# Performance work log

Measured on AMD Instinct MI355X. Metric: run time of the kernel, lower is better.

## Reference

```python
import jax, jax.numpy as jnp
import numpy as np

VOCAB = 65
N_EMBD = 32
BLOCK = 8
N_HEADS = 4
HEAD = N_EMBD // N_HEADS  # 8
SQRT_C = float(N_EMBD) ** 0.5  # faithful bug: scores are MULTIPLIED by sqrt(n_embd)


def setup_inputs() -> dict:
    key = jax.random.key(0)
    ks = jax.random.split(key, 12)
    B, T = 65536, 8
    idx = jax.random.randint(ks[0], (B, T), 0, VOCAB, dtype=jnp.int64 if jax.config.jax_enable_x64 else jnp.int32)
    targets = jax.random.randint(ks[1], (B, T), 0, VOCAB, dtype=idx.dtype)
    s = 1.0 / np.sqrt(N_EMBD)
    return {
        "idx": idx,
        "targets": targets,
        "tok_emb": jax.random.normal(ks[2], (VOCAB, N_EMBD), jnp.float32),
        "pos_emb": jax.random.normal(ks[3], (BLOCK, N_EMBD), jnp.float32),
        # per-head Q/K/V projections stacked: [n_heads, n_embd, head_size]
        "Wq": jax.random.normal(ks[4], (N_HEADS, N_EMBD, HEAD), jnp.float32) * s,
        "Wk": jax.random.normal(ks[5], (N_HEADS, N_EMBD, HEAD), jnp.float32) * s,
        "Wv": jax.random.normal(ks[6], (N_HEADS, N_EMBD, HEAD), jnp.float32) * s,
        "W_mlp": jax.random.normal(ks[7], (N_EMBD, N_EMBD), jnp.float32) * s,
        "b_mlp": jnp.zeros((N_EMBD,), jnp.float32),
        "W_lm": jax.random.normal(ks[8], (N_EMBD, VOCAB), jnp.float32) * s,
        "b_lm": jnp.zeros((VOCAB,), jnp.float32),
    }


def reference(idx, targets, tok_emb, pos_emb, Wq, Wk, Wv, W_mlp, b_mlp, W_lm, b_lm):
    B, T = idx.shape
    x = tok_emb[idx] + pos_emb[:T]                       # [B,T,C]
    q = jnp.einsum('btc,hcd->bhtd', x, Wq)               # [B,H,T,D]
    k = jnp.einsum('btc,hcd->bhtd', x, Wk)
    v = jnp.einsum('btc,hcd->bhtd', x, Wv)
    wei = jnp.einsum('bhtd,bhsd->bhts', q, k) * SQRT_C   # faithful: * C**0.5
    tril = jnp.tril(jnp.ones((T, T), bool))
    wei = jnp.where(tril, wei, -jnp.inf)
    wei = jax.nn.softmax(wei, axis=-1)
    out = jnp.einsum('bhts,bhsd->bhtd', wei, v)          # [B,H,T,D]
    x = out.transpose(0, 2, 1, 3).reshape(B, T, N_EMBD)  # concat heads
    x = jax.nn.relu(x @ W_mlp + b_mlp)                   # MLP
    logits = x @ W_lm + b_lm                             # [B,T,V]
    logits = logits.reshape(B * T, VOCAB)
    logp = jax.nn.log_softmax(logits, axis=-1)
    tgt = targets.reshape(B * T)
    loss = -jnp.take_along_axis(logp, tgt[:, None], axis=-1).mean()
    return logits, loss
```

## Files before the change

### kernel.cpp

```cpp
#include <hip/hip_runtime.h>
#include <hip/hip_bf16.h>

#define VOCAB   65
#define SQRT_C  5.656854249492381f
#define BATCHES 65536
#define ROWS    (BATCHES * 8)
#define NPAIRS  (8 * VOCAB)
#define TABSZ   (NPAIRS * 32)
#define PAIRS   (BATCHES / 2)
#define GRID    8192

__device__ __forceinline__ void wave_fence() {
    __asm__ volatile("s_waitcnt lgkmcnt(0)" ::: "memory");
}

__global__ void qkv_table_kernel(const float* __restrict__ tok_emb,
                                 const float* __restrict__ pos_emb,
                                 const float* __restrict__ Wq,
                                 const float* __restrict__ Wk,
                                 const float* __restrict__ Wv,
                                 float* __restrict__ qtab,
                                 float* __restrict__ ktab,
                                 float* __restrict__ vtab) {
    int o = blockIdx.x * 256 + threadIdx.x;
    if (o >= 3 * TABSZ) return;
    int table = o / TABSZ;
    int r = o - table * TABSZ;
    int pair = r >> 5;
    int cd = r & 31;
    int t = pair / VOCAB;
    int tok = pair - t * VOCAB;
    int h = cd >> 3, d = cd & 7;
    const float* W = (table == 0) ? Wq : (table == 1) ? Wk : Wv;
    float acc = 0.f;
    #pragma unroll
    for (int c = 0; c < 32; ++c) {
        float xc = tok_emb[tok * 32 + c] + pos_emb[t * 32 + c];
        acc += xc * W[h * 256 + c * 8 + d];
    }
    float* tab = (table == 0) ? qtab : (table == 1) ? ktab : vtab;
    tab[r] = acc;
}

__global__ __launch_bounds__(64) void fused_kernel(
        const int* __restrict__ idx, const int* __restrict__ targets,
        const float* __restrict__ qtab, const float* __restrict__ ktab,
        const float* __restrict__ vtab,
        const float* __restrict__ W_mlp,
        const float* __restrict__ b_mlp,
        const float* __restrict__ W_lm,
        const float* __restrict__ b_lm,
        float* __restrict__ out_logits,
        float* __restrict__ loss_acc) {
    __shared__ __align__(16) float sQ[576];
    __shared__ __align__(16) float sK[576];
    __shared__ __align__(16) float sV[576];
    __shared__ __align__(16) float sX2[576];
    __shared__ __align__(16) float sX3[576];
    __shared__ __align__(16) float sW64[32];

    const int l = threadIdx.x;

    if (l < 32) sW64[l] = W_lm[l * VOCAB + 64];

    const int j = l & 31;
    float wc[32], wl[32];
    #pragma unroll
    for (int c = 0; c < 32; ++c) wc[c] = W_mlp[c * 32 + j];
    #pragma unroll
    for (int c = 0; c < 32; ++c) wl[c] = W_lm[c * VOCAB + l];
    const float bm   = b_mlp[j];
    const float bl   = b_lm[l];
    const float bl64 = b_lm[64];
    wave_fence();

    float loss_local = 0.f;

    for (int pb = blockIdx.x; pb < PAIRS; pb += GRID) {
        int tokv = 0, tgv = 0;
        if (l < 16) { tokv = idx[pb * 16 + l]; tgv = targets[pb * 16 + l]; }

        {
            int t = l >> 3, c4 = l & 7;
            int h = c4 >> 1;
            int la = h * 72 + t * 8 + (c4 & 1) * 4;
            #pragma unroll
            for (int b2 = 0; b2 < 2; ++b2) {
                int tok_t = __shfl(tokv, b2 * 8 + t);
                int base = (t * VOCAB + tok_t) * 32 + c4 * 4;
                int laddr = b2 * 288 + la;
                *(float4*)(sQ + laddr) = *(const float4*)(qtab + base);
                *(float4*)(sK + laddr) = *(const float4*)(ktab + base);
                *(float4*)(sV + laddr) = *(const float4*)(vtab + base);
            }
        }
        wave_fence();

        {
            int b2 = l >> 5, h = (l >> 3) & 3, t = l & 7;
            int hb = b2 * 288 + h * 72;
            const float4 q0 = *(const float4*)(sQ + hb + t * 8);
            const float4 q1 = *(const float4*)(sQ + hb + t * 8 + 4);
            float sc[8], m = -1e30f;
            #pragma unroll
            for (int s = 0; s < 8; ++s) {
                float4 k0 = *(const float4*)(sK + hb + s * 8);
                float4 k1 = *(const float4*)(sK + hb + s * 8 + 4);
                float d = q0.x * k0.x + q0.y * k0.y + q0.z * k0.z + q0.w * k0.w
                        + q1.x * k1.x + q1.y * k1.y + q1.z * k1.z + q1.w * k1.w;
                d *= SQRT_C;
                sc[s] = d;
                if (s <= t) m = fmaxf(m, d);
            }
            float p[8], sum = 0.f;
            #pragma unroll
            for (int s = 0; s < 8; ++s) {
                p[s] = (s <= t) ? __expf(sc[s] - m) : 0.f;
                sum += p[s];
            }
            float inv = 1.f / sum;
            float o0x = 0, o0y = 0, o0z = 0, o0w = 0, o1x = 0, o1y = 0, o1z = 0, o1w = 0;
            #pragma unroll
            for (int s = 0; s < 8; ++s) {
                float4 v0 = *(const float4*)(sV + hb + s * 8);
                float4 v1 = *(const float4*)(sV + hb + s * 8 + 4);
                o0x += p[s] * v0.x; o0y += p[s] * v0.y; o0z += p[s] * v0.z; o0w += p[s] * v0.w;
                o1x += p[s] * v1.x; o1y += p[s] * v1.y; o1z += p[s] * v1.z; o1w += p[s] * v1.w;
            }
            int xb = b2 * 288 + t * 36 + h * 8;
            *(float4*)(sX2 + xb)     = make_float4(o0x * inv, o0y * inv, o0z * inv, o0w * inv);
            *(float4*)(sX2 + xb + 4) = make_float4(o1x * inv, o1y * inv, o1z * inv, o1w * inv);
        }
        wave_fence();

        #pragma unroll
        for (int i = 0; i < 8; ++i) {
            int flat = i * 64 + l;
            int b2 = flat >> 8, t = (flat >> 5) & 7;
            int xb = b2 * 288 + t * 36;
            float acc = bm;
            #pragma unroll
            for (int c4 = 0; c4 < 8; ++c4) {
                float4 xv = *(const float4*)(sX2 + xb + c4 * 4);
                acc += xv.x * wc[c4 * 4 + 0] + xv.y * wc[c4 * 4 + 1]
                     + xv.z * wc[c4 * 4 + 2] + xv.w * wc[c4 * 4 + 3];
            }
            sX3[b2 * 288 + t * 36 + j] = fmaxf(acc, 0.f);
        }
        wave_fence();

        float L64own;
        {
            int rr = l & 15;
            int xb = (rr >> 3) * 288 + (rr & 7) * 36;
            float acc = bl64;
            #pragma unroll
            for (int c4 = 0; c4 < 8; ++c4) {
                float4 xv = *(const float4*)(sX3 + xb + c4 * 4);
                float4 wv = *(const float4*)(sW64 + c4 * 4);
                acc += xv.x * wv.x + xv.y * wv.y + xv.z * wv.z + xv.w * wv.w;
            }
            L64own = acc;
        }
        if (l < 16) out_logits[(size_t)(pb * 16 + l) * VOCAB + 64] = L64own;

        #pragma unroll
        for (int g = 0; g < 2; ++g) {
            float Lr[8];
            #pragma unroll
            for (int r = 0; r < 8; ++r) {
                int xb = g * 288 + r * 36;
                float acc = bl;
                #pragma unroll
                for (int c4 = 0; c4 < 8; ++c4) {
                    float4 xv = *(const float4*)(sX3 + xb + c4 * 4);
                    acc += xv.x * wl[c4 * 4 + 0] + xv.y * wl[c4 * 4 + 1]
                         + xv.z * wl[c4 * 4 + 2] + xv.w * wl[c4 * 4 + 3];
                }
                Lr[r] = acc;
                out_logits[(size_t)(pb * 16 + g * 8 + r) * VOCAB + l] = acc;
            }
            float m[8], v64[8], ltg[8], s[8];
            #pragma unroll
            for (int r = 0; r < 8; ++r) m[r] = Lr[r];
            #pragma unroll
            for (int off = 1; off < 64; off <<= 1) {
                #pragma unroll
                for (int r = 0; r < 8; ++r) m[r] = fmaxf(m[r], __shfl_xor(m[r], off));
            }
            #pragma unroll
            for (int r = 0; r < 8; ++r) {
                v64[r] = __shfl(L64own, g * 8 + r);
                m[r] = fmaxf(m[r], v64[r]);
            }
            #pragma unroll
            for (int r = 0; r < 8; ++r) {
                int tg = __shfl(tgv, g * 8 + r);
                ltg[r] = (tg == 64) ? v64[r] : __shfl(Lr[r], tg);
            }
            #pragma unroll
            for (int r = 0; r < 8; ++r) s[r] = __expf(Lr[r] - m[r]);
            #pragma unroll
            for (int off = 1; off < 64; off <<= 1) {
                #pragma unroll
                for (int r = 0; r < 8; ++r) s[r] += __shfl_xor(s[r], off);
            }
            #pragma unroll
            for (int r = 0; r < 8; ++r) {
                s[r] += __expf(v64[r] - m[r]);
                loss_local += m[r] + __logf(s[r]) - ltg[r];
            }
        }
    }

    if (l == 0) atomicAdd(loss_acc, loss_local);
}

__global__ void finalize_loss(const float* __restrict__ acc,
                              float* __restrict__ out) {
    out[0] = acc[0] * (1.f / (float)ROWS);
}

extern "C" void kernel_launch(void* const* d_in, const int* in_sizes, int n_in,
                              void* d_out, int out_size, void* d_ws, size_t ws_size,
                              hipStream_t stream) {
    const int* idx        = (const int*)d_in[0];
    const int* targets    = (const int*)d_in[1];
    const float* tok_emb  = (const float*)d_in[2];
    const float* pos_emb  = (const float*)d_in[3];
    const float* Wq       = (const float*)d_in[4];
    const float* Wk       = (const float*)d_in[5];
    const float* Wv       = (const float*)d_in[6];
    const float* W_mlp    = (const float*)d_in[7];
    const float* b_mlp    = (const float*)d_in[8];
    const float* W_lm     = (const float*)d_in[9];
    const float* b_lm     = (const float*)d_in[10];
    float* out            = (float*)d_out;

    float* ws       = (float*)d_ws;
    float* loss_ptr = ws;
    float* qtab     = ws + 16;
    float* ktab     = qtab + TABSZ;
    float* vtab     = ktab + TABSZ;

    hipMemsetAsync(loss_ptr, 0, sizeof(float), stream);

    qkv_table_kernel<<<(3 * TABSZ + 255) / 256, 256, 0, stream>>>(
        tok_emb, pos_emb, Wq, Wk, Wv, qtab, ktab, vtab);

    fused_kernel<<<GRID, 64, 0, stream>>>(
        idx, targets, qtab, ktab, vtab, W_mlp, b_mlp, W_lm, b_lm, out, loss_ptr);

    finalize_loss<<<1, 1, 0, stream>>>(loss_ptr, out + (size_t)ROWS * VOCAB);
}
```

Measured before the change: 369.7 us.

## Use bf16 MFMA for MLP and LM head with four waves per block

Replaces the scalar FP32 MLP and LM-head matmuls with 16x16x32 bf16 MFMA instructions. Weights are held as bf16 fragments in registers, and the target logit is computed by an extra MFMA rather than through shuffles. The log-softmax drops the max subtraction and uses a 16-lane reduction. Blocks now hold four independent waves with per-wave shared buffers, and Q is read directly from global memory. The costs are reduced precision in the logits and possible overflow in the exp sum without max stabilisation.

```diff
diff --git a/kernel.cpp b/kernel.cpp
--- a/kernel.cpp
+++ b/kernel.cpp
@@ -5,13 +5,20 @@
 #define SQRT_C  5.656854249492381f
 #define BATCHES 65536
 #define ROWS    (BATCHES * 8)
-#define NPAIRS  (8 * VOCAB)
-#define TABSZ   (NPAIRS * 32)
+#define TABSZ   (8 * VOCAB * 32)
 #define PAIRS   (BATCHES / 2)
-#define GRID    8192
+#define NBLOCKS 2048
+#define NWAVES  (NBLOCKS * 4)
+
+typedef __attribute__((ext_vector_type(8))) short  short8;
+typedef __attribute__((ext_vector_type(4))) float  float4v;
 
 __device__ __forceinline__ void wave_fence() {
     __asm__ volatile("s_waitcnt lgkmcnt(0)" ::: "memory");
+}
+__device__ __forceinline__ short bfbits(float f) {
+    __hip_bfloat16 h = __float2bfloat16(f);
+    return *reinterpret_cast<short*>(&h);
 }
 
 __global__ void qkv_table_kernel(const float* __restrict__ tok_emb,
@@ -42,7 +49,7 @@
     tab[r] = acc;
 }
 
-__global__ __launch_bounds__(64) void fused_kernel(
+__global__ __launch_bounds__(256) void fused_kernel(
         const int* __restrict__ idx, const int* __restrict__ targets,
         const float* __restrict__ qtab, const float* __restrict__ ktab,
         const float* __restrict__ vtab,
@@ -52,167 +59,152 @@
         const float* __restrict__ b_lm,
         float* __restrict__ out_logits,
         float* __restrict__ loss_acc) {
-    __shared__ __align__(16) float sQ[576];
-    __shared__ __align__(16) float sK[576];
-    __shared__ __align__(16) float sV[576];
-    __shared__ __align__(16) float sX2[576];
-    __shared__ __align__(16) float sX3[576];
-    __shared__ __align__(16) float sW64[32];
-
-    const int l = threadIdx.x;
-
-    if (l < 32) sW64[l] = W_lm[l * VOCAB + 64];
-
-    const int j = l & 31;
-    float wc[32], wl[32];
-    #pragma unroll
-    for (int c = 0; c < 32; ++c) wc[c] = W_mlp[c * 32 + j];
-    #pragma unroll
-    for (int c = 0; c < 32; ++c) wl[c] = W_lm[c * VOCAB + l];
-    const float bm   = b_mlp[j];
-    const float bl   = b_lm[l];
+    __shared__ __align__(16) float sK[4][544];
+    __shared__ __align__(16) float sV[4][544];
+    __shared__ __align__(16) unsigned short sX3[4][640];
+
+    const int tid = threadIdx.x;
+    const int w = tid >> 6, l = tid & 63;
+    const int q4 = l >> 4;
+    const int n  = l & 15;
+    const int t  = l & 7, b2 = (l >> 3) & 1, h = q4;
+
+    short8 wmf[2], wlf[4], wlf4;
+    #pragma unroll
+    for (int c = 0; c < 2; ++c)
+        #pragma unroll
+        for (int j = 0; j < 8; ++j)
+            wmf[c][j] = bfbits(W_mlp[(q4 * 8 + j) * 32 + c * 16 + n]);
+    #pragma unroll
+    for (int c = 0; c < 4; ++c)
+        #pragma unroll
+        for (int j = 0; j < 8; ++j)
+            wlf[c][j] = bfbits(W_lm[(q4 * 8 + j) * VOCAB + c * 16 + n]);
+    #pragma unroll
+    for (int j = 0; j < 8; ++j)
+        wlf4[j] = (n == 0) ? bfbits(W_lm[(q4 * 8 + j) * VOCAB + 64]) : (short)0;
+    float bmc[2], blc[4];
+    #pragma unroll
+    for (int c = 0; c < 2; ++c) bmc[c] = b_mlp[c * 16 + n];
+    #pragma unroll
+    for (int c = 0; c < 4; ++c) blc[c] = b_lm[c * 16 + n];
     const float bl64 = b_lm[64];
-    wave_fence();
+    const float4v zf = {0.f, 0.f, 0.f, 0.f};
 
     float loss_local = 0.f;
 
-    for (int pb = blockIdx.x; pb < PAIRS; pb += GRID) {
+    for (int pb = blockIdx.x * 4 + w; pb < PAIRS; pb += NWAVES) {
         int tokv = 0, tgv = 0;
         if (l < 16) { tokv = idx[pb * 16 + l]; tgv = targets[pb * 16 + l]; }
 
-        {
-            int t = l >> 3, c4 = l & 7;
-            int h = c4 >> 1;
-            int la = h * 72 + t * 8 + (c4 & 1) * 4;
+        #pragma unroll
+        for (int half = 0; half < 2; ++half) {
+            int c = l + half * 64;
+            int d2 = c & 1, s = (c >> 1) & 7, grp = c >> 4;
+            int b2g = grp & 1, hg = grp >> 1;
+            int tok_s = __shfl(tokv, b2g * 8 + s);
+            int gaddr = (s * VOCAB + tok_s) * 32 + hg * 8 + d2 * 4;
+            int laddr = grp * 68 + s * 8 + d2 * 4;
+            *(float4*)(&sK[w][laddr]) = *(const float4*)(ktab + gaddr);
+            *(float4*)(&sV[w][laddr]) = *(const float4*)(vtab + gaddr);
+        }
+        int tok_t = __shfl(tokv, b2 * 8 + t);
+        const float* qp = qtab + (t * VOCAB + tok_t) * 32 + h * 8;
+        const float4 q0 = *(const float4*)(qp);
+        const float4 q1 = *(const float4*)(qp + 4);
+        wave_fence();
+
+        const float* kb = &sK[w][(h * 2 + b2) * 68];
+        const float* vb = &sV[w][(h * 2 + b2) * 68];
+        float sc[8], m = -1e30f;
+        #pragma unroll
+        for (int s = 0; s < 8; ++s) {
+            float4 k0 = *(const float4*)(kb + s * 8);
+            float4 k1 = *(const float4*)(kb + s * 8 + 4);
+            float d = q0.x * k0.x + q0.y * k0.y + q0.z * k0.z + q0.w * k0.w
+                    + q1.x * k1.x + q1.y * k1.y + q1.z * k1.z + q1.w * k1.w;
+            d *= SQRT_C;
+            sc[s] = d;
+            if (s <= t) m = fmaxf(m, d);
+        }
+        float p[8], sum = 0.f;
+        #pragma unroll
+        for (int s = 0; s < 8; ++s) {
+            p[s] = (s <= t) ? __expf(sc[s] - m) : 0.f;
+            sum += p[s];
+        }
+        float inv = 1.f / sum;
+        float o[8];
+        #pragma unroll
+        for (int d = 0; d < 8; ++d) o[d] = 0.f;
+        #pragma unroll
+        for (int s = 0; s < 8; ++s) {
+            float4 v0 = *(const float4*)(vb + s * 8);
+            float4 v1 = *(const float4*)(vb + s * 8 + 4);
+            o[0] += p[s] * v0.x; o[1] += p[s] * v0.y; o[2] += p[s] * v0.z; o[3] += p[s] * v0.w;
+            o[4] += p[s] * v1.x; o[5] += p[s] * v1.y; o[6] += p[s] * v1.z; o[7] += p[s] * v1.w;
+        }
+        short8 a2;
+        #pragma unroll
+        for (int d = 0; d < 8; ++d) a2[d] = bfbits(o[d] * inv);
+
+        float4v d0 = __builtin_amdgcn_mfma_f32_16x16x32_bf16(a2, wmf[0], zf, 0, 0, 0);
+        float4v d1 = __builtin_amdgcn_mfma_f32_16x16x32_bf16(a2, wmf[1], zf, 0, 0, 0);
+        #pragma unroll
+        for (int i = 0; i < 4; ++i) {
+            int row = q4 * 4 + i;
+            sX3[w][row * 40 + n]      = (unsigned short)bfbits(fmaxf(d0[i] + bmc[0], 0.f));
+            sX3[w][row * 40 + 16 + n] = (unsigned short)bfbits(fmaxf(d1[i] + bmc[1], 0.f));
+        }
+        wave_fence();
+        short8 a3 = *(const short8*)(&sX3[w][n * 40 + q4 * 8]);
+
+        int tgn = __shfl(tgv, n);
+        short8 b6;
+        #pragma unroll
+        for (int j = 0; j < 8; ++j) b6[j] = bfbits(W_lm[(q4 * 8 + j) * VOCAB + tgn]);
+        float btg = b_lm[tgn];
+
+        float4v Lc[4];
+        #pragma unroll
+        for (int c = 0; c < 4; ++c)
+            Lc[c] = __builtin_amdgcn_mfma_f32_16x16x32_bf16(a3, wlf[c], zf, 0, 0, 0);
+        float4v L64 = __builtin_amdgcn_mfma_f32_16x16x32_bf16(a3, wlf4, zf, 0, 0, 0);
+        float4v Ltg = __builtin_amdgcn_mfma_f32_16x16x32_bf16(a3, b6, zf, 0, 0, 0);
+
+        size_t rb = (size_t)pb * 16;
+        float part[4] = {0.f, 0.f, 0.f, 0.f};
+        #pragma unroll
+        for (int c = 0; c < 4; ++c) {
             #pragma unroll
-            for (int b2 = 0; b2 < 2; ++b2) {
-                int tok_t = __shfl(tokv, b2 * 8 + t);
-                int base = (t * VOCAB + tok_t) * 32 + c4 * 4;
-                int laddr = b2 * 288 + la;
-                *(float4*)(sQ + laddr) = *(const float4*)(qtab + base);
-                *(float4*)(sK + laddr) = *(const float4*)(ktab + base);
-                *(float4*)(sV + laddr) = *(const float4*)(vtab + base);
+            for (int i = 0; i < 4; ++i) {
+                float Lv = Lc[c][i] + blc[c];
+                out_logits[(rb + q4 * 4 + i) * VOCAB + c * 16 + n] = Lv;
+                part[i] += __expf(Lv);
             }
         }
-        wave_fence();
-
-        {
-            int b2 = l >> 5, h = (l >> 3) & 3, t = l & 7;
-            int hb = b2 * 288 + h * 72;
-            const float4 q0 = *(const float4*)(sQ + hb + t * 8);
-            const float4 q1 = *(const float4*)(sQ + hb + t * 8 + 4);
-            float sc[8], m = -1e30f;
+        if (n == 0) {
             #pragma unroll
-            for (int s = 0; s < 8; ++s) {
-                float4 k0 = *(const float4*)(sK + hb + s * 8);
-                float4 k1 = *(const float4*)(sK + hb + s * 8 + 4);
-                float d = q0.x * k0.x + q0.y * k0.y + q0.z * k0.z + q0.w * k0.w
-                        + q1.x * k1.x + q1.y * k1.y + q1.z * k1.z + q1.w * k1.w;
-                d *= SQRT_C;
-                sc[s] = d;
-                if (s <= t) m = fmaxf(m, d);
+            for (int i = 0; i < 4; ++i) {
+                float Lv = L64[i] + bl64;
+                out_logits[(rb + q4 * 4 + i) * VOCAB + 64] = Lv;
+                part[i] += __expf(Lv);
             }
-            float p[8], sum = 0.f;
+        }
+        #pragma unroll
+        for (int off = 1; off < 16; off <<= 1) {
             #pragma unroll
-            for (int s = 0; s < 8; ++s) {
-                p[s] = (s <= t) ? __expf(sc[s] - m) : 0.f;
-                sum += p[s];
-            }
-            float inv = 1.f / sum;
-            float o0x = 0, o0y = 0, o0z = 0, o0w = 0, o1x = 0, o1y = 0, o1z = 0, o1w = 0;
-            #pragma unroll
-            for (int s = 0; s < 8; ++s) {
-                float4 v0 = *(const float4*)(sV + hb + s * 8);
-                float4 v1 = *(const float4*)(sV + hb + s * 8 + 4);
-                o0x += p[s] * v0.x; o0y += p[s] * v0.y; o0z += p[s] * v0.z; o0w += p[s] * v0.w;
-                o1x += p[s] * v1.x; o1y += p[s] * v1.y; o1z += p[s] * v1.z; o1w += p[s] * v1.w;
-            }
-            int xb = b2 * 288 + t * 36 + h * 8;
-            *(float4*)(sX2 + xb)     = make_float4(o0x * inv, o0y * inv, o0z * inv, o0w * inv);
-            *(float4*)(sX2 + xb + 4) = make_float4(o1x * inv, o1y * inv, o1z * inv, o1w * inv);
-        }
-        wave_fence();
-
-        #pragma unroll
-        for (int i = 0; i < 8; ++i) {
-            int flat = i * 64 + l;
-            int b2 = flat >> 8, t = (flat >> 5) & 7;
-            int xb = b2 * 288 + t * 36;
-            float acc = bm;
-            #pragma unroll
-            for (int c4 = 0; c4 < 8; ++c4) {
-                float4 xv = *(const float4*)(sX2 + xb + c4 * 4);
-                acc += xv.x * wc[c4 * 4 + 0] + xv.y * wc[c4 * 4 + 1]
-                     + xv.z * wc[c4 * 4 + 2] + xv.w * wc[c4 * 4 + 3];
-            }
-            sX3[b2 * 288 + t * 36 + j] = fmaxf(acc, 0.f);
-        }
-        wave_fence();
-
-        float L64own;
-        {
-            int rr = l & 15;
-            int xb = (rr >> 3) * 288 + (rr & 7) * 36;
-            float acc = bl64;
-            #pragma unroll
-            for (int c4 = 0; c4 < 8; ++c4) {
-                float4 xv = *(const float4*)(sX3 + xb + c4 * 4);
-                float4 wv = *(const float4*)(sW64 + c4 * 4);
-                acc += xv.x * wv.x + xv.y * wv.y + xv.z * wv.z + xv.w * wv.w;
-            }
-            L64own = acc;
-        }
-        if (l < 16) out_logits[(size_t)(pb * 16 + l) * VOCAB + 64] = L64own;
-
-        #pragma unroll
-        for (int g = 0; g < 2; ++g) {
-            float Lr[8];
-            #pragma unroll
-            for (int r = 0; r < 8; ++r) {
-                int xb = g * 288 + r * 36;
-                float acc = bl;
-                #pragma unroll
-                for (int c4 = 0; c4 < 8; ++c4) {
-                    float4 xv = *(const float4*)(sX3 + xb + c4 * 4);
-                    acc += xv.x * wl[c4 * 4 + 0] + xv.y * wl[c4 * 4 + 1]
-                         + xv.z * wl[c4 * 4 + 2] + xv.w * wl[c4 * 4 + 3];
-                }
-                Lr[r] = acc;
-                out_logits[(size_t)(pb * 16 + g * 8 + r) * VOCAB + l] = acc;
-            }
-            float m[8], v64[8], ltg[8], s[8];
-            #pragma unroll
-            for (int r = 0; r < 8; ++r) m[r] = Lr[r];
-            #pragma unroll
-            for (int off = 1; off < 64; off <<= 1) {
-                #pragma unroll
-                for (int r = 0; r < 8; ++r) m[r] = fmaxf(m[r], __shfl_xor(m[r], off));
-            }
-            #pragma unroll
-            for (int r = 0; r < 8; ++r) {
-                v64[r] = __shfl(L64own, g * 8 + r);
-                m[r] = fmaxf(m[r], v64[r]);
-            }
-            #pragma unroll
-            for (int r = 0; r < 8; ++r) {
-                int tg = __shfl(tgv, g * 8 + r);
-                ltg[r] = (tg == 64) ? v64[r] : __shfl(Lr[r], tg);
-            }
-            #pragma unroll
-            for (int r = 0; r < 8; ++r) s[r] = __expf(Lr[r] - m[r]);
-            #pragma unroll
-            for (int off = 1; off < 64; off <<= 1) {
-                #pragma unroll
-                for (int r = 0; r < 8; ++r) s[r] += __shfl_xor(s[r], off);
-            }
-            #pragma unroll
-            for (int r = 0; r < 8; ++r) {
-                s[r] += __expf(v64[r] - m[r]);
-                loss_local += m[r] + __logf(s[r]) - ltg[r];
-            }
-        }
+            for (int i = 0; i < 4; ++i) part[i] += __shfl_xor(part[i], off);
+        }
+        float lg = __logf(part[0]) + __logf(part[1]) + __logf(part[2]) + __logf(part[3]);
+        if (n == 0) loss_local += lg;
+        int rd = n - q4 * 4;
+        float tval = (rd == 0) ? Ltg[0] : (rd == 1) ? Ltg[1] : (rd == 2) ? Ltg[2] : Ltg[3];
+        if (rd >= 0 && rd <= 3) loss_local -= (tval + btg);
     }
 
+    #pragma unroll
+    for (int off = 1; off < 64; off <<= 1) loss_local += __shfl_xor(loss_local, off);
     if (l == 0) atomicAdd(loss_acc, loss_local);
 }
 
@@ -248,7 +240,7 @@
     qkv_table_kernel<<<(3 * TABSZ + 255) / 256, 256, 0, stream>>>(
         tok_emb, pos_emb, Wq, Wk, Wv, qtab, ktab, vtab);
 
-    fused_kernel<<<GRID, 64, 0, stream>>>(
+    fused_kernel<<<NBLOCKS, 256, 0, stream>>>(
         idx, targets, qtab, ktab, vtab, W_mlp, b_mlp, W_lm, b_lm, out, loss_ptr);
 
     finalize_loss<<<1, 1, 0, stream>>>(loss_ptr, out + (size_t)ROWS * VOCAB);
```

Measured after the change: 313.6 us. 1.18x faster.
